# Kernel optimization log

Hardware: AMD Instinct MI355X
Metric: run time of the kernel (lower is better)

## Reference

```python
import math
import jax, jax.numpy as jnp
import numpy as np

B, L, D = 8, 4096, 512
FACTOR = 5


def setup_inputs() -> dict:
    key = jax.random.key(0)
    kq, kk, kv = jax.random.split(key, 3)
    q = jax.random.normal(kq, (B, L, D), dtype=jnp.float32)
    k = jax.random.normal(kk, (B, L, D), dtype=jnp.float32)
    v = jax.random.normal(kv, (B, L, D), dtype=jnp.float32)
    return {"q": q, "k": k, "v": v}


def reference(q, k, v):
    # ProbSparse attention (sparse=True branch, L_Q > 1)
    L_Q = q.shape[1]
    scale = q.shape[-1] ** -0.5
    # scores: [B, L_Q, L_K]
    scores = jnp.einsum('bqd,bkd->bqk', q, k) * scale
    # sparsity measure M = max - mean over keys: [B, L_Q]
    M = scores.max(axis=-1) - scores.mean(axis=-1)
    u = max(1, int(FACTOR * math.log(L_Q + 1)))
    u = min(u, L_Q)  # static python int (u = 41 here)
    _, top_idx = jax.lax.top_k(M, u)  # [B, u]
    # gather top-u query rows of scores, softmax over keys (row-wise softmax
    # commutes with row selection, so this matches softmax-then-gather)
    scores_top = jnp.take_along_axis(scores, top_idx[:, :, None], axis=1)  # [B, u, L_K]
    attn = jax.nn.softmax(scores_top, axis=-1)
    out_top = jnp.einsum('buk,bkd->bud', attn, v)  # [B, u, D]
    # non-selected queries receive the mean value
    v_mean = jnp.broadcast_to(v.mean(axis=1, keepdims=True), v.shape)  # [B, L, D]
    b_idx = jnp.arange(q.shape[0])[:, None]  # [B, 1]
    out = v_mean.at[b_idx, top_idx].set(out_top)
    return out
```

## Files before the change

kernel.cpp:

```cpp
#include <hip/hip_runtime.h>
#include <math.h>

#define B_ 8
#define L_ 4096
#define D_ 512
#define U_ 41
#define NSL 32

static constexpr float SCALE = 0.044194173824159216f;

typedef __attribute__((ext_vector_type(8))) short bf16x8;
typedef __attribute__((ext_vector_type(4))) float f32x4;
typedef unsigned int uint;

__device__ inline uint bf16_rne_bits(float x) {
  uint u = __builtin_bit_cast(uint, x);
  return (u + 0x7FFFu + ((u >> 16) & 1u)) >> 16;
}
__device__ inline float bits_to_f32(uint hi16) {
  return __builtin_bit_cast(float, hi16 << 16);
}

__global__ __launch_bounds__(256) void kSumKV(const float* __restrict__ k,
                                              const float* __restrict__ v,
                                              unsigned char* __restrict__ dhi,
                                              unsigned char* __restrict__ dlo,
                                              float* __restrict__ partk,
                                              float* __restrict__ partv) {
  const int rt = blockIdx.x;
  const int b = blockIdx.y;
  const int tid = threadIdx.x;
  const int rg = tid >> 6;
  const int c = tid & 63;
  const int dsi = c >> 3, c16 = c & 7;
  const int d = c * 8;

  const size_t kbase = ((size_t)(b * L_ + rt * 128 + rg * 32)) * D_ + d;
  const size_t dstBase = (size_t)b * 4194304 + (size_t)rt * 131072 +
                         (size_t)dsi * 16384 + (uint)((c16 << 4) ^ 0);

  float ks[8] = {0.f, 0.f, 0.f, 0.f, 0.f, 0.f, 0.f, 0.f};
  float vs[8] = {0.f, 0.f, 0.f, 0.f, 0.f, 0.f, 0.f, 0.f};

  for (int i = 0; i < 32; ++i) {
    const int row = rg * 32 + i;
    float x[8];
    *(float4*)(x) = *(const float4*)(k + kbase + (size_t)i * D_);
    *(float4*)(x + 4) = *(const float4*)(k + kbase + (size_t)i * D_ + 4);
    uint hw[4], lw[4];
#pragma unroll
    for (int p = 0; p < 4; ++p) {
      float a = x[2 * p], cc = x[2 * p + 1];
      uint ha = bf16_rne_bits(a), hc = bf16_rne_bits(cc);
      float ra = a - bits_to_f32(ha);
      float rc = cc - bits_to_f32(hc);
      uint la = bf16_rne_bits(ra), lc = bf16_rne_bits(rc);
      hw[p] = ha | (hc << 16);
      lw[p] = la | (lc << 16);
    }
    const size_t dstByte = (size_t)b * 4194304 + (size_t)rt * 131072 +
                           (size_t)dsi * 16384 + (size_t)row * 128 +
                           (uint)((c16 << 4) ^ ((row & 7) << 4));
    *(uint4*)(dhi + dstByte) = make_uint4(hw[0], hw[1], hw[2], hw[3]);
    *(uint4*)(dlo + dstByte) = make_uint4(lw[0], lw[1], lw[2], lw[3]);
#pragma unroll
    for (int e = 0; e < 8; ++e) ks[e] += x[e];

    float y[8];
    *(float4*)(y) = *(const float4*)(v + kbase + (size_t)i * D_);
    *(float4*)(y + 4) = *(const float4*)(v + kbase + (size_t)i * D_ + 4);
#pragma unroll
    for (int e = 0; e < 8; ++e) vs[e] += y[e];
  }
  const size_t pb = ((size_t)(b * 128 + rt * 4 + rg)) * D_ + d;
  *(float4*)(partk + pb) = *(float4*)(ks);
  *(float4*)(partk + pb + 4) = *(float4*)(ks + 4);
  *(float4*)(partv + pb) = *(float4*)(vs);
  *(float4*)(partv + pb + 4) = *(float4*)(vs + 4);
}

__global__ __launch_bounds__(512) void kSums2V(const float* __restrict__ partk,
                                               const float* __restrict__ partv,
                                               float* __restrict__ ksum,
                                               float* __restrict__ vmean) {
  const int b = blockIdx.x;
  const int d = threadIdx.x;
  float ks = 0.f, vs = 0.f;
  for (int p = 0; p < 128; ++p) {
    ks += partk[((size_t)(b * 128 + p)) * D_ + d];
    vs += partv[((size_t)(b * 128 + p)) * D_ + d];
  }
  ksum[b * D_ + d] = ks;
  vmean[b * D_ + d] = vs * (1.f / L_);
}

__global__ __launch_bounds__(512) void kSums1(const float* __restrict__ k,
                                              const float* __restrict__ v,
                                              float* __restrict__ partk,
                                              float* __restrict__ partv) {
  const int s = blockIdx.x;
  const int b = blockIdx.y;
  const int d = threadIdx.x;
  const int rows = L_ / NSL;
  const size_t base = ((size_t)b * L_ + (size_t)s * rows) * D_ + d;
  float ks = 0.f, vs = 0.f;
  for (int l = 0; l < rows; ++l) {
    ks += k[base + (size_t)l * D_];
    vs += v[base + (size_t)l * D_];
  }
  partk[(b * NSL + s) * D_ + d] = ks;
  partv[(b * NSL + s) * D_ + d] = vs;
}

__global__ __launch_bounds__(512) void kSums2(const float* __restrict__ partk,
                                              const float* __restrict__ partv,
                                              float* __restrict__ ksum,
                                              float* __restrict__ vmean) {
  const int b = blockIdx.x;
  const int d = threadIdx.x;
  float ks = 0.f, vs = 0.f;
  for (int s = 0; s < NSL; ++s) {
    ks += partk[(b * NSL + s) * D_ + d];
    vs += partv[(b * NSL + s) * D_ + d];
  }
  ksum[b * D_ + d] = ks;
  vmean[b * D_ + d] = vs * (1.f / L_);
}

__global__ __launch_bounds__(256) void kMeanM(const float* __restrict__ q,
                                              const float* __restrict__ ksum,
                                              const float* __restrict__ pmax,
                                              float* __restrict__ M) {
  __shared__ float ks[D_];
  const int gid = blockIdx.x * 256 + threadIdx.x;
  const int b = gid >> 12;
  for (int i = threadIdx.x; i < D_; i += 256) ks[i] = ksum[b * D_ + i];
  __syncthreads();
  const float* qp = q + (size_t)gid * D_;
  float acc = 0.f;
  for (int i = 0; i < D_; i += 4) {
    float4 t = *(const float4*)(qp + i);
    acc += t.x * ks[i] + t.y * ks[i + 1] + t.z * ks[i + 2] + t.w * ks[i + 3];
  }
  const float rowmax = fmaxf(pmax[gid], pmax[B_ * L_ + gid]);
  M[gid] = SCALE * (rowmax - acc * (1.f / L_));
}

__global__ __launch_bounds__(256) void kTopK3(const float* __restrict__ M,
                                              int* __restrict__ topidx) {
  __shared__ float wv[2][4];
  __shared__ int wi[2][4];
  const int b = blockIdx.x;
  const int tid = threadIdx.x;
  const int wave = tid >> 6, lane = tid & 63;
  float v[16];
#pragma unroll
  for (int j = 0; j < 16; ++j) v[j] = M[b * L_ + tid + j * 256];
  float bv = v[0];
  int bj = 0;
#pragma unroll
  for (int j = 1; j < 16; ++j)
    if (v[j] > bv) { bv = v[j]; bj = j; }
  int bi = tid + bj * 256;

  for (int it = 0; it < U_; ++it) {
    float rv = bv;
    int ri = bi;
#pragma unroll
    for (int off = 1; off < 64; off <<= 1) {
      float ov = __shfl_xor(rv, off);
      int oi = __shfl_xor(ri, off);
      if (ov > rv || (ov == rv && oi < ri)) { rv = ov; ri = oi; }
    }
    const int par = it & 1;
    if (lane == 0) { wv[par][wave] = rv; wi[par][wave] = ri; }
    __syncthreads();
    float gv = wv[par][0];
    int gi = wi[par][0];
#pragma unroll
    for (int w = 1; w < 4; ++w) {
      float ov = wv[par][w];
      int oi = wi[par][w];
      if (ov > gv || (ov == gv && oi < gi)) { gv = ov; gi = oi; }
    }
    if (tid == 0) topidx[b * U_ + it] = gi;
    if (gi == bi) {
      const int jb = gi >> 8;
#pragma unroll
      for (int j = 0; j < 16; ++j)
        if (j == jb) v[j] = -3.4e38f;
      bv = v[0];
      bj = 0;
#pragma unroll
      for (int j = 1; j < 16; ++j)
        if (v[j] > bv) { bv = v[j]; bj = j; }
      bi = tid + bj * 256;
    }
  }
}

__global__ __launch_bounds__(64) void kTopK4(const float* __restrict__ pmax,
                                             const float* __restrict__ qdot,
                                             int* __restrict__ topidx) {
  const int b = blockIdx.x;
  const int lane = threadIdx.x;
  float v[64];
#pragma unroll
  for (int j = 0; j < 64; ++j) {
    const int gid = b * L_ + lane + j * 64;
    v[j] = SCALE * (fmaxf(pmax[gid], pmax[B_ * L_ + gid]) - qdot[gid] * (1.f / L_));
  }
  float bv = v[0];
  int bj = 0;
#pragma unroll
  for (int j = 1; j < 64; ++j)
    if (v[j] > bv) { bv = v[j]; bj = j; }
  int bi = lane + bj * 64;

  for (int it = 0; it < U_; ++it) {
    float rv = bv;
    int ri = bi;
#pragma unroll
    for (int off = 1; off < 64; off <<= 1) {
      float ov = __shfl_xor(rv, off);
      int oi = __shfl_xor(ri, off);
      if (ov > rv || (ov == rv && oi < ri)) { rv = ov; ri = oi; }
    }
    if (lane == 0) topidx[b * U_ + it] = ri;
    if (ri == bi) {
#pragma unroll
      for (int j = 0; j < 64; ++j)
        if (j == bj) v[j] = -3.4e38f;
      bv = v[0];
      bj = 0;
#pragma unroll
      for (int j = 1; j < 64; ++j)
        if (v[j] > bv) { bv = v[j]; bj = j; }
      bi = lane + bj * 64;
    }
  }
}

__global__ __launch_bounds__(256) void kFill(const float* __restrict__ vmean,
                                             float* __restrict__ out) {
  const int g = blockIdx.x * 256 + threadIdx.x;
  const int d4 = g & 127;
  const int bl = g >> 7;
  const int b = bl >> 12;
  ((float4*)out)[g] = ((const float4*)vmean)[b * 128 + d4];
}

__global__ __launch_bounds__(256) void kConvertQdot(const float* __restrict__ src,
                                                    const float* __restrict__ ksum,
                                                    unsigned char* __restrict__ dhi,
                                                    unsigned char* __restrict__ dlo,
                                                    float* __restrict__ qdotp) {
  const int cid = blockIdx.x * 256 + threadIdx.x;
  const int c16 = cid & 7;
  const int row = (cid >> 3) & 127;
  const int dsi = (cid >> 10) & 7;
  const int rt = (cid >> 13) & 31;
  const int b = cid >> 18;
  const int l = rt * 128 + row;
  const int d = dsi * 64 + c16 * 8;
  const float* sp = src + ((size_t)(b * L_ + l) * D_ + d);
  float x[8];
  *(float4*)(x) = *(const float4*)sp;
  *(float4*)(x + 4) = *(const float4*)(sp + 4);

  const float* kp = ksum + b * D_ + d;
  float dot = 0.f;
#pragma unroll
  for (int i = 0; i < 8; ++i) dot += x[i] * kp[i];
#pragma unroll
  for (int off = 1; off < 8; off <<= 1) dot += __shfl_xor(dot, off);

  uint hw[4], lw[4];
#pragma unroll
  for (int p = 0; p < 4; ++p) {
    float a = x[2 * p], c = x[2 * p + 1];
    uint ha = bf16_rne_bits(a), hc = bf16_rne_bits(c);
    float ra = a - bits_to_f32(ha);
    float rc = c - bits_to_f32(hc);
    uint la = bf16_rne_bits(ra), lc = bf16_rne_bits(rc);
    hw[p] = ha | (hc << 16);
    lw[p] = la | (lc << 16);
  }
  const size_t dstByte = ((size_t)(cid >> 3) << 7) +
                         (uint)((c16 << 4) ^ ((row & 7) << 4));
  *(uint4*)(dhi + dstByte) = make_uint4(hw[0], hw[1], hw[2], hw[3]);
  *(uint4*)(dlo + dstByte) = make_uint4(lw[0], lw[1], lw[2], lw[3]);
  if (c16 == 0)
    qdotp[((size_t)dsi * B_ * L_) + b * L_ + l] = dot;
}

__global__ __launch_bounds__(256) void kQdotReduce(const float* __restrict__ qdotp,
                                                   float* __restrict__ qdot) {
  const int gid = blockIdx.x * 256 + threadIdx.x;
  float s = 0.f;
#pragma unroll
  for (int i = 0; i < 8; ++i) s += qdotp[(size_t)i * B_ * L_ + gid];
  qdot[gid] = s;
}

__device__ __forceinline__ void gload16(const unsigned char* g, unsigned char* l) {
  __builtin_amdgcn_global_load_lds(
      (const __attribute__((address_space(1))) unsigned int*)(g),
      (__attribute__((address_space(3))) unsigned int*)(l), 16, 0, 0);
}

__global__ __launch_bounds__(256, 2) void kRowMaxB(const unsigned char* __restrict__ qhi,
                                                   const unsigned char* __restrict__ qlo,
                                                   const unsigned char* __restrict__ khi,
                                                   const unsigned char* __restrict__ klo,
                                                   float* __restrict__ pmax) {
  __shared__ unsigned char lds[65536];
  __shared__ float red[256];
  unsigned char* ldsQhi = lds;
  unsigned char* ldsQlo = lds + 16384;
  unsigned char* ldsKhi = lds + 32768;
  unsigned char* ldsKlo = lds + 49152;

  const int b = blockIdx.y;
  const int qt = blockIdx.x;
  const int kh = blockIdx.z;
  const int tid = threadIdx.x;
  const int lane = tid & 63;
  const int wave = tid >> 6;
  const int wq = wave >> 1, wk = wave & 1;

  const size_t qtb = ((size_t)((b * 32 + qt) * 8)) * 16384;
  const unsigned char* qhB = qhi + qtb;
  const unsigned char* qlB = qlo + qtb;

  float rmax[4][4];
#pragma unroll
  for (int i = 0; i < 4; ++i)
#pragma unroll
    for (int j = 0; j < 4; ++j) rmax[i][j] = -3.4e38f;

  for (int kt = 0; kt < 16; ++kt) {
    const size_t ktb = ((size_t)((b * 32 + (kh * 16 + kt)) * 8)) * 16384;
    const unsigned char* khB = khi + ktb;
    const unsigned char* klB = klo + ktb;

    f32x4 acc[4][4];
#pragma unroll
    for (int i = 0; i < 4; ++i)
#pragma unroll
      for (int j = 0; j < 4; ++j)
#pragma unroll
        for (int e = 0; e < 4; ++e) acc[i][j][e] = 0.f;

    for (int dsi = 0; dsi < 8; ++dsi) {
      __syncthreads();
      {
        const size_t dof = (size_t)dsi * 16384 + (size_t)tid * 16;
        const size_t lof = (size_t)tid * 16;
#pragma unroll
        for (int i = 0; i < 4; ++i) {
          gload16(qhB + dof + i * 4096, ldsQhi + lof + i * 4096);
          gload16(qlB + dof + i * 4096, ldsQlo + lof + i * 4096);
          gload16(khB + dof + i * 4096, ldsKhi + lof + i * 4096);
          gload16(klB + dof + i * 4096, ldsKlo + lof + i * 4096);
        }
      }
      __syncthreads();

#pragma unroll
      for (int h = 0; h < 2; ++h) {
        const int rbyte = h * 64 + ((lane >> 4) << 4);
        bf16x8 aH[4], aL[4], bH[4], bL[4];
#pragma unroll
        for (int f = 0; f < 4; ++f) {
          const int qrow = wq * 64 + f * 16 + (lane & 15);
          const int krow = wk * 64 + f * 16 + (lane & 15);
          const int qoff = qrow * 128 + (rbyte ^ ((qrow & 7) << 4));
          const int koff = krow * 128 + (rbyte ^ ((krow & 7) << 4));
          aH[f] = *(const bf16x8*)(ldsQhi + qoff);
          aL[f] = *(const bf16x8*)(ldsQlo + qoff);
          bH[f] = *(const bf16x8*)(ldsKhi + koff);
          bL[f] = *(const bf16x8*)(ldsKlo + koff);
        }
#pragma unroll
        for (int mf = 0; mf < 4; ++mf)
#pragma unroll
          for (int nf = 0; nf < 4; ++nf) {
            acc[mf][nf] = __builtin_amdgcn_mfma_f32_16x16x32_bf16(aH[mf], bH[nf], acc[mf][nf], 0, 0, 0);
            acc[mf][nf] = __builtin_amdgcn_mfma_f32_16x16x32_bf16(aH[mf], bL[nf], acc[mf][nf], 0, 0, 0);
            acc[mf][nf] = __builtin_amdgcn_mfma_f32_16x16x32_bf16(aL[mf], bH[nf], acc[mf][nf], 0, 0, 0);
          }
      }
    }
#pragma unroll
    for (int mf = 0; mf < 4; ++mf)
#pragma unroll
      for (int r = 0; r < 4; ++r) {
        float m = fmaxf(fmaxf(acc[mf][0][r], acc[mf][1][r]),
                        fmaxf(acc[mf][2][r], acc[mf][3][r]));
        rmax[mf][r] = fmaxf(rmax[mf][r], m);
      }
  }

#pragma unroll
  for (int mf = 0; mf < 4; ++mf)
#pragma unroll
    for (int r = 0; r < 4; ++r) {
      float v = rmax[mf][r];
#pragma unroll
      for (int off = 1; off < 16; off <<= 1) v = fmaxf(v, __shfl_xor(v, off));
      rmax[mf][r] = v;
    }

  if ((lane & 15) == 0) {
#pragma unroll
    for (int mf = 0; mf < 4; ++mf)
#pragma unroll
      for (int r = 0; r < 4; ++r) {
        const int rowl = wq * 64 + mf * 16 + ((lane >> 4) << 2) + r;
        red[wk * 128 + rowl] = rmax[mf][r];
      }
  }
  __syncthreads();
  if (tid < 128) {
    pmax[(size_t)kh * B_ * L_ + (size_t)b * L_ + qt * 128 + tid] =
        fmaxf(red[tid], red[128 + tid]);
  }
}


__global__ __launch_bounds__(64) void kGatherQ(const float* __restrict__ q,
                                               const int* __restrict__ topidx,
                                               unsigned char* __restrict__ qselhi,
                                               unsigned char* __restrict__ qsello) {
  const int j = blockIdx.x;
  const int b = blockIdx.y;
  const int lane = threadIdx.x;
  const int dsi = lane >> 3;
  const int c16 = lane & 7;
  float x[8] = {0.f, 0.f, 0.f, 0.f, 0.f, 0.f, 0.f, 0.f};
  if (j < U_) {
    const int row = topidx[b * U_ + j];
    const float* sp = q + ((size_t)(b * L_ + row)) * D_ + dsi * 64 + c16 * 8;
    *(float4*)(x) = *(const float4*)sp;
    *(float4*)(x + 4) = *(const float4*)(sp + 4);
  }
  uint hw[4], lw[4];
#pragma unroll
  for (int p = 0; p < 4; ++p) {
    float a = x[2 * p], c = x[2 * p + 1];
    uint ha = bf16_rne_bits(a), hc = bf16_rne_bits(c);
    float ra = a - bits_to_f32(ha);
    float rc = c - bits_to_f32(hc);
    uint la = bf16_rne_bits(ra), lc = bf16_rne_bits(rc);
    hw[p] = ha | (hc << 16);
    lw[p] = la | (lc << 16);
  }
  const size_t dstByte = ((size_t)((b * 8 + dsi) * 64 + j)) * 128 +
                         (uint)((c16 << 4) ^ ((j & 7) << 4));
  *(uint4*)(qselhi + dstByte) = make_uint4(hw[0], hw[1], hw[2], hw[3]);
  *(uint4*)(qsello + dstByte) = make_uint4(lw[0], lw[1], lw[2], lw[3]);
}

__global__ __launch_bounds__(256) void kSelScoresM(const unsigned char* __restrict__ qselhi,
                                                   const unsigned char* __restrict__ qsello,
                                                   const unsigned char* __restrict__ khi,
                                                   const unsigned char* __restrict__ klo,
                                                   float* __restrict__ P) {
  __shared__ unsigned char lds[49152];
  unsigned char* ldsQhi = lds;
  unsigned char* ldsQlo = lds + 8192;
  unsigned char* ldsKhi = lds + 16384;
  unsigned char* ldsKlo = lds + 32768;

  const int kc = blockIdx.x;
  const int b = blockIdx.y;
  const int tid = threadIdx.x;
  const int lane = tid & 63;
  const int wave = tid >> 6;
  const int wq = wave >> 1, wk = wave & 1;

  const size_t ktb = ((size_t)((b * 32 + kc) * 8)) * 16384;
  const unsigned char* khB = khi + ktb;
  const unsigned char* klB = klo + ktb;
  const size_t qb = ((size_t)b * 8) * 8192;
  const unsigned char* qhB = qselhi + qb;
  const unsigned char* qlB = qsello + qb;

  f32x4 acc[2][4];
#pragma unroll
  for (int i = 0; i < 2; ++i)
#pragma unroll
    for (int j = 0; j < 4; ++j)
#pragma unroll
      for (int e = 0; e < 4; ++e) acc[i][j][e] = 0.f;

  for (int dsi = 0; dsi < 8; ++dsi) {
    __syncthreads();
    {
      const size_t qof = (size_t)dsi * 8192 + (size_t)tid * 16;
      const size_t kof = (size_t)dsi * 16384 + (size_t)tid * 16;
      const size_t lof = (size_t)tid * 16;
#pragma unroll
      for (int i = 0; i < 2; ++i) {
        gload16(qhB + qof + i * 4096, ldsQhi + lof + i * 4096);
        gload16(qlB + qof + i * 4096, ldsQlo + lof + i * 4096);
      }
#pragma unroll
      for (int i = 0; i < 4; ++i) {
        gload16(khB + kof + i * 4096, ldsKhi + lof + i * 4096);
        gload16(klB + kof + i * 4096, ldsKlo + lof + i * 4096);
      }
    }
    __syncthreads();

#pragma unroll
    for (int h = 0; h < 2; ++h) {
      const int rbyte = h * 64 + ((lane >> 4) << 4);
      bf16x8 aH[2], aL[2], bH[4], bL[4];
#pragma unroll
      for (int f = 0; f < 2; ++f) {
        const int qrow = wq * 32 + f * 16 + (lane & 15);
        const int qoff = qrow * 128 + (rbyte ^ ((qrow & 7) << 4));
        aH[f] = *(const bf16x8*)(ldsQhi + qoff);
        aL[f] = *(const bf16x8*)(ldsQlo + qoff);
      }
#pragma unroll
      for (int f = 0; f < 4; ++f) {
        const int krow = wk * 64 + f * 16 + (lane & 15);
        const int koff = krow * 128 + (rbyte ^ ((krow & 7) << 4));
        bH[f] = *(const bf16x8*)(ldsKhi + koff);
        bL[f] = *(const bf16x8*)(ldsKlo + koff);
      }
#pragma unroll
      for (int mf = 0; mf < 2; ++mf)
#pragma unroll
        for (int nf = 0; nf < 4; ++nf) {
          acc[mf][nf] = __builtin_amdgcn_mfma_f32_16x16x32_bf16(aH[mf], bH[nf], acc[mf][nf], 0, 0, 0);
          acc[mf][nf] = __builtin_amdgcn_mfma_f32_16x16x32_bf16(aH[mf], bL[nf], acc[mf][nf], 0, 0, 0);
          acc[mf][nf] = __builtin_amdgcn_mfma_f32_16x16x32_bf16(aL[mf], bH[nf], acc[mf][nf], 0, 0, 0);
        }
    }
  }

#pragma unroll
  for (int mf = 0; mf < 2; ++mf)
#pragma unroll
    for (int nf = 0; nf < 4; ++nf)
#pragma unroll
      for (int r = 0; r < 4; ++r) {
        const int row = wq * 32 + mf * 16 + ((lane >> 4) << 2) + r;
        const int key = kc * 128 + wk * 64 + nf * 16 + (lane & 15);
        if (row < U_)
          P[((size_t)(b * U_ + row)) * L_ + key] = acc[mf][nf][r];
      }
}

__global__ __launch_bounds__(256) void kSoftmaxP(float* __restrict__ P) {
  __shared__ float red[256];
  const int j = blockIdx.x, b = blockIdx.y;
  float* row = P + ((size_t)(b * U_ + j)) * L_;
  const int tid = threadIdx.x;
  float v[16];
  float mx = -3.4e38f;
#pragma unroll
  for (int i = 0; i < 16; ++i) {
    v[i] = row[tid + i * 256];
    mx = fmaxf(mx, v[i]);
  }
  red[tid] = mx;
  __syncthreads();
  for (int s = 128; s > 0; s >>= 1) {
    if (tid < s) red[tid] = fmaxf(red[tid], red[tid + s]);
    __syncthreads();
  }
  mx = red[0];
  __syncthreads();
  float sum = 0.f;
#pragma unroll
  for (int i = 0; i < 16; ++i) {
    float e = expf((v[i] - mx) * SCALE);
    v[i] = e;
    sum += e;
  }
  red[tid] = sum;
  __syncthreads();
  for (int s = 128; s > 0; s >>= 1) {
    if (tid < s) red[tid] += red[tid + s];
    __syncthreads();
  }
  const float inv = 1.f / red[0];
#pragma unroll
  for (int i = 0; i < 16; ++i) row[tid + i * 256] = v[i] * inv;
}

__global__ __launch_bounds__(256) void kPV(const float* __restrict__ P,
                                           const float* __restrict__ v,
                                           float* __restrict__ partial) {
  __shared__ float plds[41 * 128];
  const int kc = blockIdx.x;
  const int dc = blockIdx.y;
  const int b = blockIdx.z;
  const int tid = threadIdx.x;
  const int trow = tid >> 7, dcol = tid & 127;
  float acc[U_];
#pragma unroll
  for (int j = 0; j < U_; ++j) acc[j] = 0.f;

  for (int sub = 0; sub < 4; ++sub) {
    const int key0 = kc * 512 + sub * 128;
    __syncthreads();
    for (int idx = tid; idx < U_ * 128; idx += 256)
      plds[idx] = P[((size_t)(b * U_ + (idx >> 7))) * L_ + key0 + (idx & 127)];
    __syncthreads();
    const float* vp = v + ((size_t)(b * L_ + key0 + trow * 64)) * D_ + dc * 128 + dcol;
    float vv[64];
#pragma unroll
    for (int kk = 0; kk < 64; ++kk) vv[kk] = vp[(size_t)kk * D_];
#pragma unroll
    for (int j = 0; j < U_; ++j) {
      const float4* pr = (const float4*)&plds[j * 128 + trow * 64];
      float a = acc[j];
#pragma unroll
      for (int q4 = 0; q4 < 16; ++q4) {
        float4 p4 = pr[q4];
        a = fmaf(p4.x, vv[q4 * 4 + 0], a);
        a = fmaf(p4.y, vv[q4 * 4 + 1], a);
        a = fmaf(p4.z, vv[q4 * 4 + 2], a);
        a = fmaf(p4.w, vv[q4 * 4 + 3], a);
      }
      acc[j] = a;
    }
  }
  float* pp = partial + ((size_t)((b * 4 + dc) * 16 + kc * 2 + trow)) * (U_ * 128) + dcol;
#pragma unroll
  for (int j = 0; j < U_; ++j) pp[j * 128] = acc[j];
}

__global__ __launch_bounds__(256) void kPVout(const float* __restrict__ partial,
                                              const int* __restrict__ topidx,
                                              float* __restrict__ out) {
  const int j = blockIdx.x, b = blockIdx.y;
  const int tid = threadIdx.x;
  const int l = topidx[b * U_ + j];
#pragma unroll
  for (int h = 0; h < 2; ++h) {
    const int d = tid + h * 256;
    const int dc = d >> 7, dcol = d & 127;
    float s = 0.f;
#pragma unroll
    for (int part = 0; part < 16; ++part)
      s += partial[((size_t)((b * 4 + dc) * 16 + part)) * (U_ * 128) + j * 128 + dcol];
    out[((size_t)(b * L_ + l)) * D_ + d] = s;
  }
}


__device__ inline void stageHalfRow(const float* __restrict__ src,
                                    char* hiBase, char* loBase,
                                    int row, int shalf) {
  const int sw = (row & 7) << 4;
  char* hp = hiBase + row * 128;
  char* lp = loBase + row * 128;
#pragma unroll
  for (int g = 0; g < 4; ++g) {
    f32x4 x0 = *(const f32x4*)(src + g * 8);
    f32x4 x1 = *(const f32x4*)(src + g * 8 + 4);
    float x[8] = {x0.x, x0.y, x0.z, x0.w, x1.x, x1.y, x1.z, x1.w};
    uint hw[4], lw[4];
#pragma unroll
    for (int p = 0; p < 4; ++p) {
      float a = x[2 * p], c = x[2 * p + 1];
      uint ha = bf16_rne_bits(a), hc = bf16_rne_bits(c);
      float ra = a - bits_to_f32(ha);
      float rc = c - bits_to_f32(hc);
      uint la = bf16_rne_bits(ra), lc = bf16_rne_bits(rc);
      hw[p] = ha | (hc << 16);
      lw[p] = la | (lc << 16);
    }
    const int off = (shalf * 64 + g * 16) ^ sw;
    *(uint4*)(hp + off) = make_uint4(hw[0], hw[1], hw[2], hw[3]);
    *(uint4*)(lp + off) = make_uint4(lw[0], lw[1], lw[2], lw[3]);
  }
}

__global__ __launch_bounds__(256, 2) void kRowMaxM(const float* __restrict__ q,
                                                   const float* __restrict__ k,
                                                   float* __restrict__ pmax) {
  __shared__ char lds[65536];
  __shared__ float red[256];
  char* ldsQhi = lds;
  char* ldsQlo = lds + 16384;
  char* ldsKhi = lds + 32768;
  char* ldsKlo = lds + 49152;

  const int b = blockIdx.y;
  const int qbase = blockIdx.x * 128;
  const int kh = blockIdx.z;
  const int tid = threadIdx.x;
  const int lane = tid & 63;
  const int wave = tid >> 6;
  const int wq = wave >> 1, wk = wave & 1;
  const int srow = tid >> 1;
  const int shalf = tid & 1;

  const float* qrow_base = q + ((size_t)b * L_ + qbase + srow) * D_ + shalf * 32;
  const float* krow_base = k + ((size_t)b * L_ + kh * 2048 + srow) * D_ + shalf * 32;

  float rmax[4][4];
#pragma unroll
  for (int i = 0; i < 4; ++i)
#pragma unroll
    for (int j = 0; j < 4; ++j) rmax[i][j] = -3.4e38f;

  for (int kt = 0; kt < 16; ++kt) {
    f32x4 acc[4][4];
#pragma unroll
    for (int i = 0; i < 4; ++i)
#pragma unroll
      for (int j = 0; j < 4; ++j)
#pragma unroll
        for (int e = 0; e < 4; ++e) acc[i][j][e] = 0.f;

    for (int dsi = 0; dsi < 8; ++dsi) {
      __syncthreads();
      stageHalfRow(qrow_base + dsi * 64, ldsQhi, ldsQlo, srow, shalf);
      stageHalfRow(krow_base + (size_t)kt * 128 * D_ + dsi * 64, ldsKhi, ldsKlo, srow, shalf);
      __syncthreads();

#pragma unroll
      for (int h = 0; h < 2; ++h) {
        const int rbyte = h * 64 + ((lane >> 4) << 4);
        bf16x8 aH[4], aL[4], bH[4], bL[4];
#pragma unroll
        for (int f = 0; f < 4; ++f) {
          const int qrow = wq * 64 + f * 16 + (lane & 15);
          const int krow = wk * 64 + f * 16 + (lane & 15);
          const int qoff = qrow * 128 + (rbyte ^ ((qrow & 7) << 4));
          const int koff = krow * 128 + (rbyte ^ ((krow & 7) << 4));
          aH[f] = *(const bf16x8*)(ldsQhi + qoff);
          aL[f] = *(const bf16x8*)(ldsQlo + qoff);
          bH[f] = *(const bf16x8*)(ldsKhi + koff);
          bL[f] = *(const bf16x8*)(ldsKlo + koff);
        }
#pragma unroll
        for (int mf = 0; mf < 4; ++mf)
#pragma unroll
          for (int nf = 0; nf < 4; ++nf) {
            acc[mf][nf] = __builtin_amdgcn_mfma_f32_16x16x32_bf16(aH[mf], bH[nf], acc[mf][nf], 0, 0, 0);
            acc[mf][nf] = __builtin_amdgcn_mfma_f32_16x16x32_bf16(aH[mf], bL[nf], acc[mf][nf], 0, 0, 0);
            acc[mf][nf] = __builtin_amdgcn_mfma_f32_16x16x32_bf16(aL[mf], bH[nf], acc[mf][nf], 0, 0, 0);
          }
      }
    }
#pragma unroll
    for (int mf = 0; mf < 4; ++mf)
#pragma unroll
      for (int r = 0; r < 4; ++r) {
        float m = fmaxf(fmaxf(acc[mf][0][r], acc[mf][1][r]),
                        fmaxf(acc[mf][2][r], acc[mf][3][r]));
        rmax[mf][r] = fmaxf(rmax[mf][r], m);
      }
  }

#pragma unroll
  for (int mf = 0; mf < 4; ++mf)
#pragma unroll
    for (int r = 0; r < 4; ++r) {
      float v = rmax[mf][r];
#pragma unroll
      for (int off = 1; off < 16; off <<= 1) v = fmaxf(v, __shfl_xor(v, off));
      rmax[mf][r] = v;
    }

  if ((lane & 15) == 0) {
#pragma unroll
    for (int mf = 0; mf < 4; ++mf)
#pragma unroll
      for (int r = 0; r < 4; ++r) {
        const int rowl = wq * 64 + mf * 16 + ((lane >> 4) << 2) + r;
        red[wk * 128 + rowl] = rmax[mf][r];
      }
  }
  __syncthreads();
  if (tid < 128) {
    pmax[(size_t)kh * B_ * L_ + (size_t)b * L_ + qbase + tid] =
        fmaxf(red[tid], red[128 + tid]);
  }
}

__global__ __launch_bounds__(256) void kAttnSel(const float* __restrict__ q,
                                                const float* __restrict__ k,
                                                const float* __restrict__ v,
                                                const int* __restrict__ topidx,
                                                float* __restrict__ out) {
  __shared__ float qs[D_];
  __shared__ float sc[L_];
  __shared__ float wred[4];
  __shared__ float sred[256];
  const int b = blockIdx.y;
  const int l_sel = topidx[b * U_ + blockIdx.x];
  const int tid = threadIdx.x;
  const int wave = tid >> 6, lane = tid & 63;
  const float* qrow = q + ((size_t)b * L_ + l_sel) * D_;
  qs[tid] = qrow[tid];
  qs[tid + 256] = qrow[tid + 256];
  __syncthreads();
  float qr[8];
#pragma unroll
  for (int i = 0; i < 8; ++i) qr[i] = qs[lane * 8 + i];
  float wmax = -3.4e38f;
  for (int l = wave; l < L_; l += 4) {
    const float* kp = k + ((size_t)b * L_ + l) * D_ + lane * 8;
    float4 k0 = *(const float4*)kp;
    float4 k1 = *(const float4*)(kp + 4);
    float p = k0.x * qr[0] + k0.y * qr[1] + k0.z * qr[2] + k0.w * qr[3] +
              k1.x * qr[4] + k1.y * qr[5] + k1.z * qr[6] + k1.w * qr[7];
#pragma unroll
    for (int off = 32; off > 0; off >>= 1) p += __shfl_xor(p, off);
    if (lane == 0) sc[l] = p;
    wmax = fmaxf(wmax, p);
  }
  if (lane == 0) wred[wave] = wmax;
  __syncthreads();
  const float mx = fmaxf(fmaxf(wred[0], wred[1]), fmaxf(wred[2], wred[3]));
  float psum = 0.f;
  for (int i = tid; i < L_; i += 256) {
    float e = expf((sc[i] - mx) * SCALE);
    sc[i] = e;
    psum += e;
  }
  sred[tid] = psum;
  __syncthreads();
  for (int s = 128; s > 0; s >>= 1) {
    if (tid < s) sred[tid] += sred[tid + s];
    __syncthreads();
  }
  const float inv = 1.f / sred[0];
  float a0a = 0.f, a0b = 0.f, a1a = 0.f, a1b = 0.f;
  const float* vb = v + (size_t)b * L_ * D_;
  for (int l = 0; l < L_; l += 2) {
    float p0 = sc[l], p1 = sc[l + 1];
    const float* vp0 = vb + (size_t)l * D_;
    const float* vp1 = vp0 + D_;
    a0a = fmaf(p0, vp0[tid], a0a);
    a1a = fmaf(p0, vp0[tid + 256], a1a);
    a0b = fmaf(p1, vp1[tid], a0b);
    a1b = fmaf(p1, vp1[tid + 256], a1b);
  }
  float* orow = out + ((size_t)b * L_ + l_sel) * D_;
  orow[tid] = (a0a + a0b) * inv;
  orow[tid + 256] = (a1a + a1b) * inv;
}


extern "C" void kernel_launch(void* const* d_in, const int* in_sizes, int n_in,
                              void* d_out, int out_size, void* d_ws, size_t ws_size,
                              hipStream_t stream) {
  const float* q = (const float*)d_in[0];
  const float* k = (const float*)d_in[1];
  const float* v = (const float*)d_in[2];
  float* out = (float*)d_out;
  unsigned char* wsb = (unsigned char*)d_ws;

  const size_t NEED = 71731200;

  if (ws_size >= NEED) {
    unsigned char* qhiW = wsb;
    unsigned char* qloW = wsb + 33554432;
    float* P = (float*)wsb;
    float* partial = (float*)(wsb + 5373952);
    unsigned char* qselhi = wsb + 16121856;
    unsigned char* qsello = wsb + 16646144;
    float* pmax = (float*)(wsb + 67108864);
    float* qdot = (float*)(wsb + 67371008);
    float* ksum = (float*)(wsb + 67502080);
    float* vmean = (float*)(wsb + 67518464);
    int* tidx = (int*)(wsb + 67534848);
    float* partk = (float*)(wsb + 67536896);
    float* partv = (float*)(wsb + 69634048);
    float* qdotp = partk;

    unsigned char* khiO = (unsigned char*)d_out;
    unsigned char* kloO = khiO + 33554432;

    kSumKV<<<dim3(32, B_), 256, 0, stream>>>(k, v, khiO, kloO, partk, partv);
    kSums2V<<<B_, 512, 0, stream>>>(partk, partv, ksum, vmean);
    kConvertQdot<<<8192, 256, 0, stream>>>(q, ksum, qhiW, qloW, qdotp);
    kQdotReduce<<<B_ * L_ / 256, 256, 0, stream>>>(qdotp, qdot);
    kRowMaxB<<<dim3(32, B_, 2), 256, 0, stream>>>(qhiW, qloW, khiO, kloO, pmax);
    kTopK4<<<B_, 64, 0, stream>>>(pmax, qdot, tidx);
    kGatherQ<<<dim3(64, B_), 64, 0, stream>>>(q, tidx, qselhi, qsello);
    kSelScoresM<<<dim3(32, B_), 256, 0, stream>>>(qselhi, qsello, khiO, kloO, P);
    kSoftmaxP<<<dim3(U_, B_), 256, 0, stream>>>(P);
    kFill<<<B_ * L_ * D_ / 1024, 256, 0, stream>>>(vmean, out);
    kPV<<<dim3(8, 4, B_), 256, 0, stream>>>(P, v, partial);
    kPVout<<<dim3(U_, B_), 256, 0, stream>>>(partial, tidx, out);
  } else {
    float* ws = (float*)d_ws;
    float* Marr = ws;
    float* pmax = ws + 32768;
    float* ksum = ws + 98304;
    float* vmean = ws + 102400;
    int* tidx = (int*)(ws + 106496);
    float* partk = ws + 107008;
    float* partv = ws + 107008 + B_ * NSL * D_;

    kSums1<<<dim3(NSL, B_), 512, 0, stream>>>(k, v, partk, partv);
    kSums2<<<B_, 512, 0, stream>>>(partk, partv, ksum, vmean);
    kRowMaxM<<<dim3(L_ / 128, B_, 2), 256, 0, stream>>>(q, k, pmax);
    kMeanM<<<B_ * L_ / 256, 256, 0, stream>>>(q, ksum, pmax, Marr);
    kTopK3<<<B_, 256, 0, stream>>>(Marr, tidx);
    kFill<<<B_ * L_ * D_ / 1024, 256, 0, stream>>>(vmean, out);
    kAttnSel<<<dim3(U_, B_), 256, 0, stream>>>(q, k, v, tidx, out);
  }
}
```

Measured before the change: 594.6 us.

## Screen row-max with bf16-only pass, then rescore top candidates at split precision

The full row-max pass over all queries now uses only the high bf16 half of Q and K, with one MFMA per tile instead of three, and Q is no longer written out as a low-bf16 residual. A candidate set of at least 41 and up to 128 queries near the top-u threshold is then rescored at hi/lo split precision. That pass also produces the scores reused for the final top-k, softmax and PV, so the separate selected-scores kernel is dropped. The risk is that a true top-u query falls outside the candidate window (fixed margin of 0.05) and is missed, and the candidate pass does extra work on up to 128 rows.

New measurement: 632.8 us. +6.4%, slower.

```diff
diff --git a/kernel.cpp b/kernel.cpp
--- a/kernel.cpp
+++ b/kernel.cpp
@@ -6,6 +6,8 @@
 #define D_ 512
 #define U_ 41
 #define NSL 32
+#define NCAND 128
+#define CANDWIN 0.05f
 
 static constexpr float SCALE = 0.044194173824159216f;
 
@@ -36,8 +38,6 @@
   const int d = c * 8;
 
   const size_t kbase = ((size_t)(b * L_ + rt * 128 + rg * 32)) * D_ + d;
-  const size_t dstBase = (size_t)b * 4194304 + (size_t)rt * 131072 +
-                         (size_t)dsi * 16384 + (uint)((c16 << 4) ^ 0);
 
   float ks[8] = {0.f, 0.f, 0.f, 0.f, 0.f, 0.f, 0.f, 0.f};
   float vs[8] = {0.f, 0.f, 0.f, 0.f, 0.f, 0.f, 0.f, 0.f};
@@ -93,6 +93,512 @@
   ksum[b * D_ + d] = ks;
   vmean[b * D_ + d] = vs * (1.f / L_);
 }
+
+__global__ __launch_bounds__(256) void kConvertHQdot(const float* __restrict__ src,
+                                                     const float* __restrict__ ksum,
+                                                     unsigned char* __restrict__ dhi,
+                                                     float* __restrict__ qdotp) {
+  const int cid = blockIdx.x * 256 + threadIdx.x;
+  const int c16 = cid & 7;
+  const int row = (cid >> 3) & 127;
+  const int dsi = (cid >> 10) & 7;
+  const int rt = (cid >> 13) & 31;
+  const int b = cid >> 18;
+  const int l = rt * 128 + row;
+  const int d = dsi * 64 + c16 * 8;
+  const float* sp = src + ((size_t)(b * L_ + l) * D_ + d);
+  float x[8];
+  *(float4*)(x) = *(const float4*)sp;
+  *(float4*)(x + 4) = *(const float4*)(sp + 4);
+
+  const float* kp = ksum + b * D_ + d;
+  float dot = 0.f;
+#pragma unroll
+  for (int i = 0; i < 8; ++i) dot += x[i] * kp[i];
+#pragma unroll
+  for (int off = 1; off < 8; off <<= 1) dot += __shfl_xor(dot, off);
+
+  uint hw[4];
+#pragma unroll
+  for (int p = 0; p < 4; ++p) {
+    float a = x[2 * p], c = x[2 * p + 1];
+    hw[p] = bf16_rne_bits(a) | (bf16_rne_bits(c) << 16);
+  }
+  const size_t dstByte = ((size_t)(cid >> 3) << 7) +
+                         (uint)((c16 << 4) ^ ((row & 7) << 4));
+  *(uint4*)(dhi + dstByte) = make_uint4(hw[0], hw[1], hw[2], hw[3]);
+  if (c16 == 0)
+    qdotp[((size_t)dsi * B_ * L_) + b * L_ + l] = dot;
+}
+
+__global__ __launch_bounds__(256) void kQdotReduce(const float* __restrict__ qdotp,
+                                                   float* __restrict__ qdot) {
+  const int gid = blockIdx.x * 256 + threadIdx.x;
+  float s = 0.f;
+#pragma unroll
+  for (int i = 0; i < 8; ++i) s += qdotp[(size_t)i * B_ * L_ + gid];
+  qdot[gid] = s;
+}
+
+__device__ __forceinline__ void gload16(const unsigned char* g, unsigned char* l) {
+  __builtin_amdgcn_global_load_lds(
+      (const __attribute__((address_space(1))) unsigned int*)(g),
+      (__attribute__((address_space(3))) unsigned int*)(l), 16, 0, 0);
+}
+
+__global__ __launch_bounds__(256, 4) void kRowMaxH(const unsigned char* __restrict__ qhi,
+                                                   const unsigned char* __restrict__ khi,
+                                                   float* __restrict__ pmax) {
+  __shared__ unsigned char lds[32768];
+  __shared__ float red[256];
+  unsigned char* ldsQ = lds;
+  unsigned char* ldsK = lds + 16384;
+
+  const int b = blockIdx.y;
+  const int qt = blockIdx.x;
+  const int kh = blockIdx.z;
+  const int tid = threadIdx.x;
+  const int lane = tid & 63;
+  const int wave = tid >> 6;
+  const int wq = wave >> 1, wk = wave & 1;
+
+  const unsigned char* qhB = qhi + ((size_t)((b * 32 + qt) * 8)) * 16384;
+
+  float rmax[4][4];
+#pragma unroll
+  for (int i = 0; i < 4; ++i)
+#pragma unroll
+    for (int j = 0; j < 4; ++j) rmax[i][j] = -3.4e38f;
+
+  for (int kt = 0; kt < 16; ++kt) {
+    const unsigned char* khB = khi + ((size_t)((b * 32 + (kh * 16 + kt)) * 8)) * 16384;
+
+    f32x4 acc[4][4];
+#pragma unroll
+    for (int i = 0; i < 4; ++i)
+#pragma unroll
+      for (int j = 0; j < 4; ++j)
+#pragma unroll
+        for (int e = 0; e < 4; ++e) acc[i][j][e] = 0.f;
+
+    for (int dsi = 0; dsi < 8; ++dsi) {
+      __syncthreads();
+      {
+        const size_t dof = (size_t)dsi * 16384 + (size_t)tid * 16;
+        const size_t lof = (size_t)tid * 16;
+#pragma unroll
+        for (int i = 0; i < 4; ++i) {
+          gload16(qhB + dof + i * 4096, ldsQ + lof + i * 4096);
+          gload16(khB + dof + i * 4096, ldsK + lof + i * 4096);
+        }
+      }
+      __syncthreads();
+
+#pragma unroll
+      for (int h = 0; h < 2; ++h) {
+        const int rbyte = h * 64 + ((lane >> 4) << 4);
+        bf16x8 aH[4], bH[4];
+#pragma unroll
+        for (int f = 0; f < 4; ++f) {
+          const int qrow = wq * 64 + f * 16 + (lane & 15);
+          const int krow = wk * 64 + f * 16 + (lane & 15);
+          aH[f] = *(const bf16x8*)(ldsQ + qrow * 128 + (rbyte ^ ((qrow & 7) << 4)));
+          bH[f] = *(const bf16x8*)(ldsK + krow * 128 + (rbyte ^ ((krow & 7) << 4)));
+        }
+#pragma unroll
+        for (int mf = 0; mf < 4; ++mf)
+#pragma unroll
+          for (int nf = 0; nf < 4; ++nf)
+            acc[mf][nf] = __builtin_amdgcn_mfma_f32_16x16x32_bf16(aH[mf], bH[nf], acc[mf][nf], 0, 0, 0);
+      }
+    }
+#pragma unroll
+    for (int mf = 0; mf < 4; ++mf)
+#pragma unroll
+      for (int r = 0; r < 4; ++r) {
+        float m = fmaxf(fmaxf(acc[mf][0][r], acc[mf][1][r]),
+                        fmaxf(acc[mf][2][r], acc[mf][3][r]));
+        rmax[mf][r] = fmaxf(rmax[mf][r], m);
+      }
+  }
+
+#pragma unroll
+  for (int mf = 0; mf < 4; ++mf)
+#pragma unroll
+    for (int r = 0; r < 4; ++r) {
+      float v = rmax[mf][r];
+#pragma unroll
+      for (int off = 1; off < 16; off <<= 1) v = fmaxf(v, __shfl_xor(v, off));
+      rmax[mf][r] = v;
+    }
+
+  __syncthreads();
+  if ((lane & 15) == 0) {
+#pragma unroll
+    for (int mf = 0; mf < 4; ++mf)
+#pragma unroll
+      for (int r = 0; r < 4; ++r) {
+        const int rowl = wq * 64 + mf * 16 + ((lane >> 4) << 2) + r;
+        red[wk * 128 + rowl] = rmax[mf][r];
+      }
+  }
+  __syncthreads();
+  if (tid < 128) {
+    pmax[(size_t)kh * B_ * L_ + (size_t)b * L_ + qt * 128 + tid] =
+        fmaxf(red[tid], red[128 + tid]);
+  }
+}
+
+__global__ __launch_bounds__(64) void kTopCand(const float* __restrict__ pmax,
+                                               const float* __restrict__ qdot,
+                                               int* __restrict__ cidx,
+                                               int* __restrict__ ccnt) {
+  const int b = blockIdx.x;
+  const int lane = threadIdx.x;
+  float v[64];
+#pragma unroll
+  for (int j = 0; j < 64; ++j) {
+    const int gid = b * L_ + lane + j * 64;
+    v[j] = SCALE * (fmaxf(pmax[gid], pmax[B_ * L_ + gid]) - qdot[gid] * (1.f / L_));
+  }
+  float bv = v[0];
+  int bj = 0;
+#pragma unroll
+  for (int j = 1; j < 64; ++j)
+    if (v[j] > bv) { bv = v[j]; bj = j; }
+  int bi = lane + bj * 64;
+
+  float thr = -3.4e38f;
+  int cnt = 0;
+  for (int it = 0; it < NCAND; ++it) {
+    float rv = bv;
+    int ri = bi;
+#pragma unroll
+    for (int off = 1; off < 64; off <<= 1) {
+      float ov = __shfl_xor(rv, off);
+      int oi = __shfl_xor(ri, off);
+      if (ov > rv || (ov == rv && oi < ri)) { rv = ov; ri = oi; }
+    }
+    if (it == 40) thr = rv - CANDWIN;
+    if (it >= 41 && rv < thr) break;
+    if (lane == 0) cidx[b * NCAND + it] = ri;
+    cnt = it + 1;
+    if (ri == bi) {
+#pragma unroll
+      for (int j = 0; j < 64; ++j)
+        if (j == bj) v[j] = -3.4e38f;
+      bv = v[0];
+      bj = 0;
+#pragma unroll
+      for (int j = 1; j < 64; ++j)
+        if (v[j] > bv) { bv = v[j]; bj = j; }
+      bi = lane + bj * 64;
+    }
+  }
+  if (lane == 0) ccnt[b] = cnt;
+}
+
+__global__ __launch_bounds__(64) void kGatherQc(const float* __restrict__ q,
+                                                const int* __restrict__ cidx,
+                                                const int* __restrict__ ccnt,
+                                                unsigned char* __restrict__ qchi,
+                                                unsigned char* __restrict__ qclo) {
+  const int j = blockIdx.x;
+  const int b = blockIdx.y;
+  const int lane = threadIdx.x;
+  const int dsi = lane >> 3;
+  const int c16 = lane & 7;
+  float x[8] = {0.f, 0.f, 0.f, 0.f, 0.f, 0.f, 0.f, 0.f};
+  if (j < ccnt[b]) {
+    const int row = cidx[b * NCAND + j];
+    const float* sp = q + ((size_t)(b * L_ + row)) * D_ + dsi * 64 + c16 * 8;
+    *(float4*)(x) = *(const float4*)sp;
+    *(float4*)(x + 4) = *(const float4*)(sp + 4);
+  }
+  uint hw[4], lw[4];
+#pragma unroll
+  for (int p = 0; p < 4; ++p) {
+    float a = x[2 * p], c = x[2 * p + 1];
+    uint ha = bf16_rne_bits(a), hc = bf16_rne_bits(c);
+    float ra = a - bits_to_f32(ha);
+    float rc = c - bits_to_f32(hc);
+    uint la = bf16_rne_bits(ra), lc = bf16_rne_bits(rc);
+    hw[p] = ha | (hc << 16);
+    lw[p] = la | (lc << 16);
+  }
+  const size_t dstByte = ((size_t)((b * 8 + dsi) * 128 + j)) * 128 +
+                         (uint)((c16 << 4) ^ ((j & 7) << 4));
+  *(uint4*)(qchi + dstByte) = make_uint4(hw[0], hw[1], hw[2], hw[3]);
+  *(uint4*)(qclo + dstByte) = make_uint4(lw[0], lw[1], lw[2], lw[3]);
+}
+
+__global__ __launch_bounds__(256) void kCandScores(const unsigned char* __restrict__ qchi,
+                                                   const unsigned char* __restrict__ qclo,
+                                                   const unsigned char* __restrict__ khi,
+                                                   const unsigned char* __restrict__ klo,
+                                                   float* __restrict__ Pc,
+                                                   float* __restrict__ pcmax) {
+  __shared__ unsigned char lds[65536];
+  __shared__ float red[256];
+  unsigned char* ldsQhi = lds;
+  unsigned char* ldsQlo = lds + 16384;
+  unsigned char* ldsKhi = lds + 32768;
+  unsigned char* ldsKlo = lds + 49152;
+
+  const int kc = blockIdx.x;
+  const int b = blockIdx.y;
+  const int tid = threadIdx.x;
+  const int lane = tid & 63;
+  const int wave = tid >> 6;
+  const int wq = wave >> 1, wk = wave & 1;
+
+  const unsigned char* qhB = qchi + (size_t)b * 131072;
+  const unsigned char* qlB = qclo + (size_t)b * 131072;
+  const size_t ktb = ((size_t)((b * 32 + kc) * 8)) * 16384;
+  const unsigned char* khB = khi + ktb;
+  const unsigned char* klB = klo + ktb;
+
+  f32x4 acc[4][4];
+#pragma unroll
+  for (int i = 0; i < 4; ++i)
+#pragma unroll
+    for (int j = 0; j < 4; ++j)
+#pragma unroll
+      for (int e = 0; e < 4; ++e) acc[i][j][e] = 0.f;
+
+  for (int dsi = 0; dsi < 8; ++dsi) {
+    __syncthreads();
+    {
+      const size_t dof = (size_t)dsi * 16384 + (size_t)tid * 16;
+      const size_t lof = (size_t)tid * 16;
+#pragma unroll
+      for (int i = 0; i < 4; ++i) {
+        gload16(qhB + dof + i * 4096, ldsQhi + lof + i * 4096);
+        gload16(qlB + dof + i * 4096, ldsQlo + lof + i * 4096);
+        gload16(khB + dof + i * 4096, ldsKhi + lof + i * 4096);
+        gload16(klB + dof + i * 4096, ldsKlo + lof + i * 4096);
+      }
+    }
+    __syncthreads();
+
+#pragma unroll
+    for (int h = 0; h < 2; ++h) {
+      const int rbyte = h * 64 + ((lane >> 4) << 4);
+      bf16x8 aH[4], aL[4], bH[4], bL[4];
+#pragma unroll
+      for (int f = 0; f < 4; ++f) {
+        const int qrow = wq * 64 + f * 16 + (lane & 15);
+        const int krow = wk * 64 + f * 16 + (lane & 15);
+        const int qoff = qrow * 128 + (rbyte ^ ((qrow & 7) << 4));
+        const int koff = krow * 128 + (rbyte ^ ((krow & 7) << 4));
+        aH[f] = *(const bf16x8*)(ldsQhi + qoff);
+        aL[f] = *(const bf16x8*)(ldsQlo + qoff);
+        bH[f] = *(const bf16x8*)(ldsKhi + koff);
+        bL[f] = *(const bf16x8*)(ldsKlo + koff);
+      }
+#pragma unroll
+      for (int mf = 0; mf < 4; ++mf)
+#pragma unroll
+        for (int nf = 0; nf < 4; ++nf) {
+          acc[mf][nf] = __builtin_amdgcn_mfma_f32_16x16x32_bf16(aH[mf], bH[nf], acc[mf][nf], 0, 0, 0);
+          acc[mf][nf] = __builtin_amdgcn_mfma_f32_16x16x32_bf16(aH[mf], bL[nf], acc[mf][nf], 0, 0, 0);
+          acc[mf][nf] = __builtin_amdgcn_mfma_f32_16x16x32_bf16(aL[mf], bH[nf], acc[mf][nf], 0, 0, 0);
+        }
+    }
+  }
+
+  float rmax[4][4];
+#pragma unroll
+  for (int mf = 0; mf < 4; ++mf)
+#pragma unroll
+    for (int nf = 0; nf < 4; ++nf)
+#pragma unroll
+      for (int r = 0; r < 4; ++r) {
+        const int row = wq * 64 + mf * 16 + ((lane >> 4) << 2) + r;
+        const int key = kc * 128 + wk * 64 + nf * 16 + (lane & 15);
+        Pc[((size_t)(b * NCAND + row)) * L_ + key] = acc[mf][nf][r];
+      }
+#pragma unroll
+  for (int mf = 0; mf < 4; ++mf)
+#pragma unroll
+    for (int r = 0; r < 4; ++r) {
+      float m = fmaxf(fmaxf(acc[mf][0][r], acc[mf][1][r]),
+                      fmaxf(acc[mf][2][r], acc[mf][3][r]));
+#pragma unroll
+      for (int off = 1; off < 16; off <<= 1) m = fmaxf(m, __shfl_xor(m, off));
+      rmax[mf][r] = m;
+    }
+  __syncthreads();
+  if ((lane & 15) == 0) {
+#pragma unroll
+    for (int mf = 0; mf < 4; ++mf)
+#pragma unroll
+      for (int r = 0; r < 4; ++r) {
+        const int rowl = wq * 64 + mf * 16 + ((lane >> 4) << 2) + r;
+        red[wk * 128 + rowl] = rmax[mf][r];
+      }
+  }
+  __syncthreads();
+  if (tid < 128)
+    pcmax[((size_t)(b * 32 + kc)) * NCAND + tid] = fmaxf(red[tid], red[128 + tid]);
+}
+
+__global__ __launch_bounds__(64) void kTopK5(const float* __restrict__ pcmax,
+                                             const float* __restrict__ qdot,
+                                             const int* __restrict__ cidx,
+                                             const int* __restrict__ ccnt,
+                                             int* __restrict__ topidx,
+                                             int* __restrict__ cslot) {
+  const int b = blockIdx.x;
+  const int lane = threadIdx.x;
+  const int cnt = ccnt[b];
+  float m0 = -3.4e38f, m1 = -3.4e38f;
+  int r0 = 0x7fffffff, r1 = 0x7fffffff;
+  const int c0 = lane, c1 = lane + 64;
+  if (c0 < cnt) {
+    float mx = -3.4e38f;
+    for (int kc = 0; kc < 32; ++kc)
+      mx = fmaxf(mx, pcmax[((size_t)(b * 32 + kc)) * NCAND + c0]);
+    r0 = cidx[b * NCAND + c0];
+    m0 = SCALE * (mx - qdot[b * L_ + r0] * (1.f / L_));
+  }
+  if (c1 < cnt) {
+    float mx = -3.4e38f;
+    for (int kc = 0; kc < 32; ++kc)
+      mx = fmaxf(mx, pcmax[((size_t)(b * 32 + kc)) * NCAND + c1]);
+    r1 = cidx[b * NCAND + c1];
+    m1 = SCALE * (mx - qdot[b * L_ + r1] * (1.f / L_));
+  }
+  for (int it = 0; it < U_; ++it) {
+    float bv; int bs, br;
+    if (m0 > m1 || (m0 == m1 && r0 < r1)) { bv = m0; bs = c0; br = r0; }
+    else { bv = m1; bs = c1; br = r1; }
+    float rv = bv; int rs = bs, rr = br;
+#pragma unroll
+    for (int off = 1; off < 64; off <<= 1) {
+      float ov = __shfl_xor(rv, off);
+      int os = __shfl_xor(rs, off);
+      int orr = __shfl_xor(rr, off);
+      if (ov > rv || (ov == rv && orr < rr)) { rv = ov; rs = os; rr = orr; }
+    }
+    if (lane == 0) { topidx[b * U_ + it] = rr; cslot[b * U_ + it] = rs; }
+    if (rs == c0) m0 = -3.4e38f;
+    if (rs == c1) m1 = -3.4e38f;
+  }
+}
+
+__global__ __launch_bounds__(256) void kSoftmaxPc(float* __restrict__ Pc,
+                                                  const int* __restrict__ cslot) {
+  __shared__ float red[256];
+  const int j = blockIdx.x, b = blockIdx.y;
+  float* row = Pc + ((size_t)(b * NCAND + cslot[b * U_ + j])) * L_;
+  const int tid = threadIdx.x;
+  float v[16];
+  float mx = -3.4e38f;
+#pragma unroll
+  for (int i = 0; i < 16; ++i) {
+    v[i] = row[tid + i * 256];
+    mx = fmaxf(mx, v[i]);
+  }
+  red[tid] = mx;
+  __syncthreads();
+  for (int s = 128; s > 0; s >>= 1) {
+    if (tid < s) red[tid] = fmaxf(red[tid], red[tid + s]);
+    __syncthreads();
+  }
+  mx = red[0];
+  __syncthreads();
+  float sum = 0.f;
+#pragma unroll
+  for (int i = 0; i < 16; ++i) {
+    float e = expf((v[i] - mx) * SCALE);
+    v[i] = e;
+    sum += e;
+  }
+  red[tid] = sum;
+  __syncthreads();
+  for (int s = 128; s > 0; s >>= 1) {
+    if (tid < s) red[tid] += red[tid + s];
+    __syncthreads();
+  }
+  const float inv = 1.f / red[0];
+#pragma unroll
+  for (int i = 0; i < 16; ++i) row[tid + i * 256] = v[i] * inv;
+}
+
+__global__ __launch_bounds__(256) void kFill(const float* __restrict__ vmean,
+                                             float* __restrict__ out) {
+  const int g = blockIdx.x * 256 + threadIdx.x;
+  const int d4 = g & 127;
+  const int bl = g >> 7;
+  const int b = bl >> 12;
+  ((float4*)out)[g] = ((const float4*)vmean)[b * 128 + d4];
+}
+
+__global__ __launch_bounds__(256) void kPVc(const float* __restrict__ Pc,
+                                            const int* __restrict__ cslot,
+                                            const float* __restrict__ v,
+                                            float* __restrict__ partial) {
+  __shared__ float plds[41 * 128];
+  __shared__ int csl[U_];
+  const int kc = blockIdx.x;
+  const int dc = blockIdx.y;
+  const int b = blockIdx.z;
+  const int tid = threadIdx.x;
+  const int trow = tid >> 7, dcol = tid & 127;
+  if (tid < U_) csl[tid] = cslot[b * U_ + tid];
+  float acc[U_];
+#pragma unroll
+  for (int j = 0; j < U_; ++j) acc[j] = 0.f;
+
+  for (int sub = 0; sub < 4; ++sub) {
+    const int key0 = kc * 512 + sub * 128;
+    __syncthreads();
+    for (int idx = tid; idx < U_ * 128; idx += 256)
+      plds[idx] = Pc[((size_t)(b * NCAND + csl[idx >> 7])) * L_ + key0 + (idx & 127)];
+    __syncthreads();
+    const float* vp = v + ((size_t)(b * L_ + key0 + trow * 64)) * D_ + dc * 128 + dcol;
+    float vv[64];
+#pragma unroll
+    for (int kk = 0; kk < 64; ++kk) vv[kk] = vp[(size_t)kk * D_];
+#pragma unroll
+    for (int j = 0; j < U_; ++j) {
+      const float4* pr = (const float4*)&plds[j * 128 + trow * 64];
+      float a = acc[j];
+#pragma unroll
+      for (int q4 = 0; q4 < 16; ++q4) {
+        float4 p4 = pr[q4];
+        a = fmaf(p4.x, vv[q4 * 4 + 0], a);
+        a = fmaf(p4.y, vv[q4 * 4 + 1], a);
+        a = fmaf(p4.z, vv[q4 * 4 + 2], a);
+        a = fmaf(p4.w, vv[q4 * 4 + 3], a);
+      }
+      acc[j] = a;
+    }
+  }
+  float* pp = partial + ((size_t)((b * 4 + dc) * 16 + kc * 2 + trow)) * (U_ * 128) + dcol;
+#pragma unroll
+  for (int j = 0; j < U_; ++j) pp[j * 128] = acc[j];
+}
+
+__global__ __launch_bounds__(256) void kPVout(const float* __restrict__ partial,
+                                              const int* __restrict__ topidx,
+                                              float* __restrict__ out) {
+  const int j = blockIdx.x, b = blockIdx.y;
+  const int tid = threadIdx.x;
+  const int l = topidx[b * U_ + j];
+#pragma unroll
+  for (int h = 0; h < 2; ++h) {
+    const int d = tid + h * 256;
+    const int dc = d >> 7, dcol = d & 127;
+    float s = 0.f;
+#pragma unroll
+    for (int part = 0; part < 16; ++part)
+      s += partial[((size_t)((b * 4 + dc) * 16 + part)) * (U_ * 128) + j * 128 + dcol];
+    out[((size_t)(b * L_ + l)) * D_ + d] = s;
+  }
+}
+
 
 __global__ __launch_bounds__(512) void kSums1(const float* __restrict__ k,
                                               const float* __restrict__ v,
@@ -198,463 +704,6 @@
     }
   }
 }
-
-__global__ __launch_bounds__(64) void kTopK4(const float* __restrict__ pmax,
-                                             const float* __restrict__ qdot,
-                                             int* __restrict__ topidx) {
-  const int b = blockIdx.x;
-  const int lane = threadIdx.x;
-  float v[64];
-#pragma unroll
-  for (int j = 0; j < 64; ++j) {
-    const int gid = b * L_ + lane + j * 64;
-    v[j] = SCALE * (fmaxf(pmax[gid], pmax[B_ * L_ + gid]) - qdot[gid] * (1.f / L_));
-  }
-  float bv = v[0];
-  int bj = 0;
-#pragma unroll
-  for (int j = 1; j < 64; ++j)
-    if (v[j] > bv) { bv = v[j]; bj = j; }
-  int bi = lane + bj * 64;
-
-  for (int it = 0; it < U_; ++it) {
-    float rv = bv;
-    int ri = bi;
-#pragma unroll
-    for (int off = 1; off < 64; off <<= 1) {
-      float ov = __shfl_xor(rv, off);
-      int oi = __shfl_xor(ri, off);
-      if (ov > rv || (ov == rv && oi < ri)) { rv = ov; ri = oi; }
-    }
-    if (lane == 0) topidx[b * U_ + it] = ri;
-    if (ri == bi) {
-#pragma unroll
-      for (int j = 0; j < 64; ++j)
-        if (j == bj) v[j] = -3.4e38f;
-      bv = v[0];
-      bj = 0;
-#pragma unroll
-      for (int j = 1; j < 64; ++j)
-        if (v[j] > bv) { bv = v[j]; bj = j; }
-      bi = lane + bj * 64;
-    }
-  }
-}
-
-__global__ __launch_bounds__(256) void kFill(const float* __restrict__ vmean,
-                                             float* __restrict__ out) {
-  const int g = blockIdx.x * 256 + threadIdx.x;
-  const int d4 = g & 127;
-  const int bl = g >> 7;
-  const int b = bl >> 12;
-  ((float4*)out)[g] = ((const float4*)vmean)[b * 128 + d4];
-}
-
-__global__ __launch_bounds__(256) void kConvertQdot(const float* __restrict__ src,
-                                                    const float* __restrict__ ksum,
-                                                    unsigned char* __restrict__ dhi,
-                                                    unsigned char* __restrict__ dlo,
-                                                    float* __restrict__ qdotp) {
-  const int cid = blockIdx.x * 256 + threadIdx.x;
-  const int c16 = cid & 7;
-  const int row = (cid >> 3) & 127;
-  const int dsi = (cid >> 10) & 7;
-  const int rt = (cid >> 13) & 31;
-  const int b = cid >> 18;
-  const int l = rt * 128 + row;
-  const int d = dsi * 64 + c16 * 8;
-  const float* sp = src + ((size_t)(b * L_ + l) * D_ + d);
-  float x[8];
-  *(float4*)(x) = *(const float4*)sp;
-  *(float4*)(x + 4) = *(const float4*)(sp + 4);
-
-  const float* kp = ksum + b * D_ + d;
-  float dot = 0.f;
-#pragma unroll
-  for (int i = 0; i < 8; ++i) dot += x[i] * kp[i];
-#pragma unroll
-  for (int off = 1; off < 8; off <<= 1) dot += __shfl_xor(dot, off);
-
-  uint hw[4], lw[4];
-#pragma unroll
-  for (int p = 0; p < 4; ++p) {
-    float a = x[2 * p], c = x[2 * p + 1];
-    uint ha = bf16_rne_bits(a), hc = bf16_rne_bits(c);
-    float ra = a - bits_to_f32(ha);
-    float rc = c - bits_to_f32(hc);
-    uint la = bf16_rne_bits(ra), lc = bf16_rne_bits(rc);
-    hw[p] = ha | (hc << 16);
-    lw[p] = la | (lc << 16);
-  }
-  const size_t dstByte = ((size_t)(cid >> 3) << 7) +
-                         (uint)((c16 << 4) ^ ((row & 7) << 4));
-  *(uint4*)(dhi + dstByte) = make_uint4(hw[0], hw[1], hw[2], hw[3]);
-  *(uint4*)(dlo + dstByte) = make_uint4(lw[0], lw[1], lw[2], lw[3]);
-  if (c16 == 0)
-    qdotp[((size_t)dsi * B_ * L_) + b * L_ + l] = dot;
-}
-
-__global__ __launch_bounds__(256) void kQdotReduce(const float* __restrict__ qdotp,
-                                                   float* __restrict__ qdot) {
-  const int gid = blockIdx.x * 256 + threadIdx.x;
-  float s = 0.f;
-#pragma unroll
-  for (int i = 0; i < 8; ++i) s += qdotp[(size_t)i * B_ * L_ + gid];
-  qdot[gid] = s;
-}
-
-__device__ __forceinline__ void gload16(const unsigned char* g, unsigned char* l) {
-  __builtin_amdgcn_global_load_lds(
-      (const __attribute__((address_space(1))) unsigned int*)(g),
-      (__attribute__((address_space(3))) unsigned int*)(l), 16, 0, 0);
-}
-
-__global__ __launch_bounds__(256, 2) void kRowMaxB(const unsigned char* __restrict__ qhi,
-                                                   const unsigned char* __restrict__ qlo,
-                                                   const unsigned char* __restrict__ khi,
-                                                   const unsigned char* __restrict__ klo,
-                                                   float* __restrict__ pmax) {
-  __shared__ unsigned char lds[65536];
-  __shared__ float red[256];
-  unsigned char* ldsQhi = lds;
-  unsigned char* ldsQlo = lds + 16384;
-  unsigned char* ldsKhi = lds + 32768;
-  unsigned char* ldsKlo = lds + 49152;
-
-  const int b = blockIdx.y;
-  const int qt = blockIdx.x;
-  const int kh = blockIdx.z;
-  const int tid = threadIdx.x;
-  const int lane = tid & 63;
-  const int wave = tid >> 6;
-  const int wq = wave >> 1, wk = wave & 1;
-
-  const size_t qtb = ((size_t)((b * 32 + qt) * 8)) * 16384;
-  const unsigned char* qhB = qhi + qtb;
-  const unsigned char* qlB = qlo + qtb;
-
-  float rmax[4][4];
-#pragma unroll
-  for (int i = 0; i < 4; ++i)
-#pragma unroll
-    for (int j = 0; j < 4; ++j) rmax[i][j] = -3.4e38f;
-
-  for (int kt = 0; kt < 16; ++kt) {
-    const size_t ktb = ((size_t)((b * 32 + (kh * 16 + kt)) * 8)) * 16384;
-    const unsigned char* khB = khi + ktb;
-    const unsigned char* klB = klo + ktb;
-
-    f32x4 acc[4][4];
-#pragma unroll
-    for (int i = 0; i < 4; ++i)
-#pragma unroll
-      for (int j = 0; j < 4; ++j)
-#pragma unroll
-        for (int e = 0; e < 4; ++e) acc[i][j][e] = 0.f;
-
-    for (int dsi = 0; dsi < 8; ++dsi) {
-      __syncthreads();
-      {
-        const size_t dof = (size_t)dsi * 16384 + (size_t)tid * 16;
-        const size_t lof = (size_t)tid * 16;
-#pragma unroll
-        for (int i = 0; i < 4; ++i) {
-          gload16(qhB + dof + i * 4096, ldsQhi + lof + i * 4096);
-          gload16(qlB + dof + i * 4096, ldsQlo + lof + i * 4096);
-          gload16(khB + dof + i * 4096, ldsKhi + lof + i * 4096);
-          gload16(klB + dof + i * 4096, ldsKlo + lof + i * 4096);
-        }
-      }
-      __syncthreads();
-
-#pragma unroll
-      for (int h = 0; h < 2; ++h) {
-        const int rbyte = h * 64 + ((lane >> 4) << 4);
-        bf16x8 aH[4], aL[4], bH[4], bL[4];
-#pragma unroll
-        for (int f = 0; f < 4; ++f) {
-          const int qrow = wq * 64 + f * 16 + (lane & 15);
-          const int krow = wk * 64 + f * 16 + (lane & 15);
-          const int qoff = qrow * 128 + (rbyte ^ ((qrow & 7) << 4));
-          const int koff = krow * 128 + (rbyte ^ ((krow & 7) << 4));
-          aH[f] = *(const bf16x8*)(ldsQhi + qoff);
-          aL[f] = *(const bf16x8*)(ldsQlo + qoff);
-          bH[f] = *(const bf16x8*)(ldsKhi + koff);
-          bL[f] = *(const bf16x8*)(ldsKlo + koff);
-        }
-#pragma unroll
-        for (int mf = 0; mf < 4; ++mf)
-#pragma unroll
-          for (int nf = 0; nf < 4; ++nf) {
-            acc[mf][nf] = __builtin_amdgcn_mfma_f32_16x16x32_bf16(aH[mf], bH[nf], acc[mf][nf], 0, 0, 0);
-            acc[mf][nf] = __builtin_amdgcn_mfma_f32_16x16x32_bf16(aH[mf], bL[nf], acc[mf][nf], 0, 0, 0);
-            acc[mf][nf] = __builtin_amdgcn_mfma_f32_16x16x32_bf16(aL[mf], bH[nf], acc[mf][nf], 0, 0, 0);
-          }
-      }
-    }
-#pragma unroll
-    for (int mf = 0; mf < 4; ++mf)
-#pragma unroll
-      for (int r = 0; r < 4; ++r) {
-        float m = fmaxf(fmaxf(acc[mf][0][r], acc[mf][1][r]),
-                        fmaxf(acc[mf][2][r], acc[mf][3][r]));
-        rmax[mf][r] = fmaxf(rmax[mf][r], m);
-      }
-  }
-
-#pragma unroll
-  for (int mf = 0; mf < 4; ++mf)
-#pragma unroll
-    for (int r = 0; r < 4; ++r) {
-      float v = rmax[mf][r];
-#pragma unroll
-      for (int off = 1; off < 16; off <<= 1) v = fmaxf(v, __shfl_xor(v, off));
-      rmax[mf][r] = v;
-    }
-
-  if ((lane & 15) == 0) {
-#pragma unroll
-    for (int mf = 0; mf < 4; ++mf)
-#pragma unroll
-      for (int r = 0; r < 4; ++r) {
-        const int rowl = wq * 64 + mf * 16 + ((lane >> 4) << 2) + r;
-        red[wk * 128 + rowl] = rmax[mf][r];
-      }
-  }
-  __syncthreads();
-  if (tid < 128) {
-    pmax[(size_t)kh * B_ * L_ + (size_t)b * L_ + qt * 128 + tid] =
-        fmaxf(red[tid], red[128 + tid]);
-  }
-}
-
-
-__global__ __launch_bounds__(64) void kGatherQ(const float* __restrict__ q,
-                                               const int* __restrict__ topidx,
-                                               unsigned char* __restrict__ qselhi,
-                                               unsigned char* __restrict__ qsello) {
-  const int j = blockIdx.x;
-  const int b = blockIdx.y;
-  const int lane = threadIdx.x;
-  const int dsi = lane >> 3;
-  const int c16 = lane & 7;
-  float x[8] = {0.f, 0.f, 0.f, 0.f, 0.f, 0.f, 0.f, 0.f};
-  if (j < U_) {
-    const int row = topidx[b * U_ + j];
-    const float* sp = q + ((size_t)(b * L_ + row)) * D_ + dsi * 64 + c16 * 8;
-    *(float4*)(x) = *(const float4*)sp;
-    *(float4*)(x + 4) = *(const float4*)(sp + 4);
-  }
-  uint hw[4], lw[4];
-#pragma unroll
-  for (int p = 0; p < 4; ++p) {
-    float a = x[2 * p], c = x[2 * p + 1];
-    uint ha = bf16_rne_bits(a), hc = bf16_rne_bits(c);
-    float ra = a - bits_to_f32(ha);
-    float rc = c - bits_to_f32(hc);
-    uint la = bf16_rne_bits(ra), lc = bf16_rne_bits(rc);
-    hw[p] = ha | (hc << 16);
-    lw[p] = la | (lc << 16);
-  }
-  const size_t dstByte = ((size_t)((b * 8 + dsi) * 64 + j)) * 128 +
-                         (uint)((c16 << 4) ^ ((j & 7) << 4));
-  *(uint4*)(qselhi + dstByte) = make_uint4(hw[0], hw[1], hw[2], hw[3]);
-  *(uint4*)(qsello + dstByte) = make_uint4(lw[0], lw[1], lw[2], lw[3]);
-}
-
-__global__ __launch_bounds__(256) void kSelScoresM(const unsigned char* __restrict__ qselhi,
-                                                   const unsigned char* __restrict__ qsello,
-                                                   const unsigned char* __restrict__ khi,
-                                                   const unsigned char* __restrict__ klo,
-                                                   float* __restrict__ P) {
-  __shared__ unsigned char lds[49152];
-  unsigned char* ldsQhi = lds;
-  unsigned char* ldsQlo = lds + 8192;
-  unsigned char* ldsKhi = lds + 16384;
-  unsigned char* ldsKlo = lds + 32768;
-
-  const int kc = blockIdx.x;
-  const int b = blockIdx.y;
-  const int tid = threadIdx.x;
-  const int lane = tid & 63;
-  const int wave = tid >> 6;
-  const int wq = wave >> 1, wk = wave & 1;
-
-  const size_t ktb = ((size_t)((b * 32 + kc) * 8)) * 16384;
-  const unsigned char* khB = khi + ktb;
-  const unsigned char* klB = klo + ktb;
-  const size_t qb = ((size_t)b * 8) * 8192;
-  const unsigned char* qhB = qselhi + qb;
-  const unsigned char* qlB = qsello + qb;
-
-  f32x4 acc[2][4];
-#pragma unroll
-  for (int i = 0; i < 2; ++i)
-#pragma unroll
-    for (int j = 0; j < 4; ++j)
-#pragma unroll
-      for (int e = 0; e < 4; ++e) acc[i][j][e] = 0.f;
-
-  for (int dsi = 0; dsi < 8; ++dsi) {
-    __syncthreads();
-    {
-      const size_t qof = (size_t)dsi * 8192 + (size_t)tid * 16;
-      const size_t kof = (size_t)dsi * 16384 + (size_t)tid * 16;
-      const size_t lof = (size_t)tid * 16;
-#pragma unroll
-      for (int i = 0; i < 2; ++i) {
-        gload16(qhB + qof + i * 4096, ldsQhi + lof + i * 4096);
-        gload16(qlB + qof + i * 4096, ldsQlo + lof + i * 4096);
-      }
-#pragma unroll
-      for (int i = 0; i < 4; ++i) {
-        gload16(khB + kof + i * 4096, ldsKhi + lof + i * 4096);
-        gload16(klB + kof + i * 4096, ldsKlo + lof + i * 4096);
-      }
-    }
-    __syncthreads();
-
-#pragma unroll
-    for (int h = 0; h < 2; ++h) {
-      const int rbyte = h * 64 + ((lane >> 4) << 4);
-      bf16x8 aH[2], aL[2], bH[4], bL[4];
-#pragma unroll
-      for (int f = 0; f < 2; ++f) {
-        const int qrow = wq * 32 + f * 16 + (lane & 15);
-        const int qoff = qrow * 128 + (rbyte ^ ((qrow & 7) << 4));
-        aH[f] = *(const bf16x8*)(ldsQhi + qoff);
-        aL[f] = *(const bf16x8*)(ldsQlo + qoff);
-      }
-#pragma unroll
-      for (int f = 0; f < 4; ++f) {
-        const int krow = wk * 64 + f * 16 + (lane & 15);
-        const int koff = krow * 128 + (rbyte ^ ((krow & 7) << 4));
-        bH[f] = *(const bf16x8*)(ldsKhi + koff);
-        bL[f] = *(const bf16x8*)(ldsKlo + koff);
-      }
-#pragma unroll
-      for (int mf = 0; mf < 2; ++mf)
-#pragma unroll
-        for (int nf = 0; nf < 4; ++nf) {
-          acc[mf][nf] = __builtin_amdgcn_mfma_f32_16x16x32_bf16(aH[mf], bH[nf], acc[mf][nf], 0, 0, 0);
-          acc[mf][nf] = __builtin_amdgcn_mfma_f32_16x16x32_bf16(aH[mf], bL[nf], acc[mf][nf], 0, 0, 0);
-          acc[mf][nf] = __builtin_amdgcn_mfma_f32_16x16x32_bf16(aL[mf], bH[nf], acc[mf][nf], 0, 0, 0);
-        }
-    }
-  }
-
-#pragma unroll
-  for (int mf = 0; mf < 2; ++mf)
-#pragma unroll
-    for (int nf = 0; nf < 4; ++nf)
-#pragma unroll
-      for (int r = 0; r < 4; ++r) {
-        const int row = wq * 32 + mf * 16 + ((lane >> 4) << 2) + r;
-        const int key = kc * 128 + wk * 64 + nf * 16 + (lane & 15);
-        if (row < U_)
-          P[((size_t)(b * U_ + row)) * L_ + key] = acc[mf][nf][r];
-      }
-}
-
-__global__ __launch_bounds__(256) void kSoftmaxP(float* __restrict__ P) {
-  __shared__ float red[256];
-  const int j = blockIdx.x, b = blockIdx.y;
-  float* row = P + ((size_t)(b * U_ + j)) * L_;
-  const int tid = threadIdx.x;
-  float v[16];
-  float mx = -3.4e38f;
-#pragma unroll
-  for (int i = 0; i < 16; ++i) {
-    v[i] = row[tid + i * 256];
-    mx = fmaxf(mx, v[i]);
-  }
-  red[tid] = mx;
-  __syncthreads();
-  for (int s = 128; s > 0; s >>= 1) {
-    if (tid < s) red[tid] = fmaxf(red[tid], red[tid + s]);
-    __syncthreads();
-  }
-  mx = red[0];
-  __syncthreads();
-  float sum = 0.f;
-#pragma unroll
-  for (int i = 0; i < 16; ++i) {
-    float e = expf((v[i] - mx) * SCALE);
-    v[i] = e;
-    sum += e;
-  }
-  red[tid] = sum;
-  __syncthreads();
-  for (int s = 128; s > 0; s >>= 1) {
-    if (tid < s) red[tid] += red[tid + s];
-    __syncthreads();
-  }
-  const float inv = 1.f / red[0];
-#pragma unroll
-  for (int i = 0; i < 16; ++i) row[tid + i * 256] = v[i] * inv;
-}
-
-__global__ __launch_bounds__(256) void kPV(const float* __restrict__ P,
-                                           const float* __restrict__ v,
-                                           float* __restrict__ partial) {
-  __shared__ float plds[41 * 128];
-  const int kc = blockIdx.x;
-  const int dc = blockIdx.y;
-  const int b = blockIdx.z;
-  const int tid = threadIdx.x;
-  const int trow = tid >> 7, dcol = tid & 127;
-  float acc[U_];
-#pragma unroll
-  for (int j = 0; j < U_; ++j) acc[j] = 0.f;
-
-  for (int sub = 0; sub < 4; ++sub) {
-    const int key0 = kc * 512 + sub * 128;
-    __syncthreads();
-    for (int idx = tid; idx < U_ * 128; idx += 256)
-      plds[idx] = P[((size_t)(b * U_ + (idx >> 7))) * L_ + key0 + (idx & 127)];
-    __syncthreads();
-    const float* vp = v + ((size_t)(b * L_ + key0 + trow * 64)) * D_ + dc * 128 + dcol;
-    float vv[64];
-#pragma unroll
-    for (int kk = 0; kk < 64; ++kk) vv[kk] = vp[(size_t)kk * D_];
-#pragma unroll
-    for (int j = 0; j < U_; ++j) {
-      const float4* pr = (const float4*)&plds[j * 128 + trow * 64];
-      float a = acc[j];
-#pragma unroll
-      for (int q4 = 0; q4 < 16; ++q4) {
-        float4 p4 = pr[q4];
-        a = fmaf(p4.x, vv[q4 * 4 + 0], a);
-        a = fmaf(p4.y, vv[q4 * 4 + 1], a);
-        a = fmaf(p4.z, vv[q4 * 4 + 2], a);
-        a = fmaf(p4.w, vv[q4 * 4 + 3], a);
-      }
-      acc[j] = a;
-    }
-  }
-  float* pp = partial + ((size_t)((b * 4 + dc) * 16 + kc * 2 + trow)) * (U_ * 128) + dcol;
-#pragma unroll
-  for (int j = 0; j < U_; ++j) pp[j * 128] = acc[j];
-}
-
-__global__ __launch_bounds__(256) void kPVout(const float* __restrict__ partial,
-                                              const int* __restrict__ topidx,
-                                              float* __restrict__ out) {
-  const int j = blockIdx.x, b = blockIdx.y;
-  const int tid = threadIdx.x;
-  const int l = topidx[b * U_ + j];
-#pragma unroll
-  for (int h = 0; h < 2; ++h) {
-    const int d = tid + h * 256;
-    const int dc = d >> 7, dcol = d & 127;
-    float s = 0.f;
-#pragma unroll
-    for (int part = 0; part < 16; ++part)
-      s += partial[((size_t)((b * 4 + dc) * 16 + part)) * (U_ * 128) + j * 128 + dcol];
-    out[((size_t)(b * L_ + l)) * D_ + d] = s;
-  }
-}
-
 
 __device__ inline void stageHalfRow(const float* __restrict__ src,
                                     char* hiBase, char* loBase,
@@ -863,22 +912,25 @@
   float* out = (float*)d_out;
   unsigned char* wsb = (unsigned char*)d_ws;
 
-  const size_t NEED = 71731200;
+  const size_t NEED = 38183168;
 
   if (ws_size >= NEED) {
     unsigned char* qhiW = wsb;
-    unsigned char* qloW = wsb + 33554432;
-    float* P = (float*)wsb;
-    float* partial = (float*)(wsb + 5373952);
-    unsigned char* qselhi = wsb + 16121856;
-    unsigned char* qsello = wsb + 16646144;
-    float* pmax = (float*)(wsb + 67108864);
-    float* qdot = (float*)(wsb + 67371008);
-    float* ksum = (float*)(wsb + 67502080);
-    float* vmean = (float*)(wsb + 67518464);
-    int* tidx = (int*)(wsb + 67534848);
-    float* partk = (float*)(wsb + 67536896);
-    float* partv = (float*)(wsb + 69634048);
+    float* Pc = (float*)wsb;
+    unsigned char* qchi = wsb + 16777216;
+    unsigned char* qclo = wsb + 17825792;
+    float* pcmax = (float*)(wsb + 18874368);
+    float* partial = (float*)(wsb + 19922944);
+    float* pmax = (float*)(wsb + 33554432);
+    float* qdot = (float*)(wsb + 33816576);
+    float* ksum = (float*)(wsb + 33947648);
+    float* vmean = (float*)(wsb + 33964032);
+    int* cidx = (int*)(wsb + 33980416);
+    int* ccnt = (int*)(wsb + 33984512);
+    int* tidx = (int*)(wsb + 33984768);
+    int* cslot = (int*)(wsb + 33986816);
+    float* partk = (float*)(wsb + 33988864);
+    float* partv = (float*)(wsb + 36086016);
     float* qdotp = partk;
 
     unsigned char* khiO = (unsigned char*)d_out;
@@ -886,15 +938,16 @@
 
     kSumKV<<<dim3(32, B_), 256, 0, stream>>>(k, v, khiO, kloO, partk, partv);
     kSums2V<<<B_, 512, 0, stream>>>(partk, partv, ksum, vmean);
-    kConvertQdot<<<8192, 256, 0, stream>>>(q, ksum, qhiW, qloW, qdotp);
+    kConvertHQdot<<<8192, 256, 0, stream>>>(q, ksum, qhiW, qdotp);
     kQdotReduce<<<B_ * L_ / 256, 256, 0, stream>>>(qdotp, qdot);
-    kRowMaxB<<<dim3(32, B_, 2), 256, 0, stream>>>(qhiW, qloW, khiO, kloO, pmax);
-    kTopK4<<<B_, 64, 0, stream>>>(pmax, qdot, tidx);
-    kGatherQ<<<dim3(64, B_), 64, 0, stream>>>(q, tidx, qselhi, qsello);
-    kSelScoresM<<<dim3(32, B_), 256, 0, stream>>>(qselhi, qsello, khiO, kloO, P);
-    kSoftmaxP<<<dim3(U_, B_), 256, 0, stream>>>(P);
+    kRowMaxH<<<dim3(32, B_, 2), 256, 0, stream>>>(qhiW, khiO, pmax);
+    kTopCand<<<B_, 64, 0, stream>>>(pmax, qdot, cidx, ccnt);
+    kGatherQc<<<dim3(NCAND, B_), 64, 0, stream>>>(q, cidx, ccnt, qchi, qclo);
+    kCandScores<<<dim3(32, B_), 256, 0, stream>>>(qchi, qclo, khiO, kloO, Pc, pcmax);
+    kTopK5<<<B_, 64, 0, stream>>>(pcmax, qdot, cidx, ccnt, tidx, cslot);
+    kSoftmaxPc<<<dim3(U_, B_), 256, 0, stream>>>(Pc, cslot);
     kFill<<<B_ * L_ * D_ / 1024, 256, 0, stream>>>(vmean, out);
-    kPV<<<dim3(8, 4, B_), 256, 0, stream>>>(P, v, partial);
+    kPVc<<<dim3(8, 4, B_), 256, 0, stream>>>(Pc, cslot, v, partial);
     kPVout<<<dim3(U_, B_), 256, 0, stream>>>(partial, tidx, out);
   } else {
     float* ws = (float*)d_ws;
```
